# Performance work log

Measured on AMD Instinct MI355X. Metric: run time of the kernel, lower is better.

The kernel has to match this reference:

```python
import jax, jax.numpy as jnp
import numpy as np
from jax import lax

B, IN_C, DIM, HEADS, K = 8, 64, 128, 4, 3
H, W = 96, 96
HEAD_DIM = DIM // HEADS
SCALE = HEAD_DIM ** -0.5
EPS = 1e-5  # BatchNorm eps (eval mode, running_mean=0, running_var=1)


def _conv3x3(x, w):
    return lax.conv_general_dilated(x, w, (1, 1), ((1, 1), (1, 1)),
                                    dimension_numbers=('NCHW', 'OIHW', 'NCHW'))


def _cbr(x, w, g, b):
    y = _conv3x3(x, w)
    y = y * (g / jnp.sqrt(1.0 + EPS))[None, :, None, None] + b[None, :, None, None]
    return jax.nn.relu(y)


def setup_inputs() -> dict:
    key = jax.random.key(0)
    ks = jax.random.split(key, 24)
    n = lambda i, s, sc=0.05: jax.random.normal(ks[i], s, jnp.float32) * sc
    u = lambda i, s: jax.random.uniform(ks[i], s, jnp.float32, 0.5, 1.5)
    return dict(
        x=jax.random.normal(ks[0], (B, IN_C, H, W), jnp.float32),
        fg=jax.random.normal(ks[1], (B, DIM, H, W), jnp.float32),
        conv1_w=n(2, (DIM, IN_C, 3, 3)), bn1_g=u(3, (DIM,)), bn1_b=n(4, (DIM,)),
        conv2_w=n(5, (DIM, DIM, 3, 3)), bn2_g=u(6, (DIM,)), bn2_b=n(7, (DIM,)),
        v_w=n(8, (DIM, DIM)), v_b=n(9, (DIM,)),
        attn_w=n(10, (K ** 4 * HEADS, DIM)), attn_b=n(11, (K ** 4 * HEADS,)),
        proj_w=n(12, (DIM, DIM)), proj_b=n(13, (DIM,)),
        conv3_w=n(14, (DIM, DIM, 3, 3)), bn3_g=u(15, (DIM,)), bn3_b=n(16, (DIM,)),
        conv4_w=n(17, (DIM, DIM, 3, 3)), bn4_g=u(18, (DIM,)), bn4_b=n(19, (DIM,)),
    )


def reference(x, fg, conv1_w, bn1_g, bn1_b, conv2_w, bn2_g, bn2_b,
              v_w, v_b, attn_w, attn_b, proj_w, proj_b,
              conv3_w, bn3_g, bn3_b, conv4_w, bn4_g, bn4_b):
    L = H * W
    # input_cbr: two conv3x3 + BN(eval) + ReLU
    xf = _cbr(_cbr(x, conv1_w, bn1_g, bn1_b), conv2_w, bn2_g, bn2_b)  # (B,DIM,H,W)
    xh = xf.transpose(0, 2, 3, 1)                 # (B,H,W,DIM)
    fgh = fg.transpose(0, 2, 3, 1)                # (B,H,W,DIM)
    # value projection then unfold (im2col, channel-major patch ordering like torch)
    v = (xh @ v_w.T + v_b).transpose(0, 3, 1, 2)  # (B,DIM,H,W)
    patches = lax.conv_general_dilated_patches(v, (K, K), (1, 1), ((1, 1), (1, 1)))  # (B,DIM*9,H,W)
    vp = patches.reshape(B, HEADS, HEAD_DIM, K * K, L).transpose(0, 1, 4, 3, 2)  # (B,h,L,9,hd)
    # attention logits directly from fg (stride=1 -> AvgPool identity)
    attn = (fgh @ attn_w.T + attn_b).reshape(B, L, HEADS, K * K, K * K)
    attn = attn.transpose(0, 2, 1, 3, 4) * SCALE  # (B,h,L,9,9)
    attn = jax.nn.softmax(attn, axis=-1)
    # batched small matmuls: (9,9) @ (9,hd) per window
    xw = jnp.einsum('bhlpq,bhlqd->bhlpd', attn, vp)  # (B,h,L,9,hd)
    xw = xw.transpose(0, 1, 4, 3, 2).reshape(B, DIM, K, K, H, W)  # channel-major, then (kh,kw)
    # fold: overlapping scatter-add back to (H,W)
    canvas = jnp.zeros((B, DIM, H + 2, W + 2), xw.dtype)
    for ki in range(K):
        for kj in range(K):
            canvas = canvas.at[:, :, ki:ki + H, kj:kj + W].add(xw[:, :, ki, kj])
    folded = canvas[:, :, 1:H + 1, 1:W + 1]        # crop padding
    p = (folded.transpose(0, 2, 3, 1) @ proj_w.T + proj_b).transpose(0, 3, 1, 2)
    # output_cbr
    out = _cbr(_cbr(p, conv3_w, bn3_g, bn3_b), conv4_w, bn4_g, bn4_b)
    return out
```

## Files before the change

### kernel.cpp

```cpp
#include <hip/hip_runtime.h>
#include <math.h>

typedef __attribute__((ext_vector_type(8))) short short8;
typedef __attribute__((ext_vector_type(4))) float f32x4;
typedef unsigned short u16;
typedef unsigned int u32;

#define HW   96
#define LPIX 9216
static constexpr float kScale = 0.17677669529663687f;

__device__ inline u16 f2bf(float f) {
    u32 x = __float_as_uint(f);
    return (u16)((x + 0x7fffu + ((x >> 16) & 1u)) >> 16);
}
__device__ inline float bf2f(u16 v) { return __uint_as_float((u32)v << 16); }

typedef __attribute__((address_space(1))) const void gas_t;
typedef __attribute__((address_space(3))) void las_t;
__device__ __forceinline__ void g2lds16(const void* g, void* l) {
    __builtin_amdgcn_global_load_lds((gas_t*)g, (las_t*)l, 16, 0, 0);
}

template <int C>
__global__ __launch_bounds__(256) void cast_nchw_nhwc(
    const float* __restrict__ in, u16* __restrict__ out)
{
    const int y = blockIdx.x, b = blockIdx.y, tid = threadIdx.x;
    __shared__ float sT[HW * C];
    for (int i = tid; i < HW * C; i += 256) {
        int c = i / HW, xx = i - c * HW;
        sT[xx * C + c] = in[(((size_t)b * C + c) * HW + y) * HW + xx];
    }
    __syncthreads();
    for (int i = tid; i < HW * (C / 8); i += 256) {
        int c8 = i % (C / 8), xx = i / (C / 8);
        union { short8 v8; u16 u[8]; } pk;
#pragma unroll
        for (int j = 0; j < 8; ++j) pk.u[j] = f2bf(sT[xx * C + c8 * 8 + j]);
        *(short8*)&out[(((size_t)b * HW + y) * HW + xx) * C + c8 * 8] = pk.v8;
    }
}

__global__ void cast_conv_w(const float* __restrict__ w, u16* __restrict__ wp, int CIN)
{
    int n = 9 * CIN * 128;
    int i = blockIdx.x * 256 + threadIdx.x;
    if (i >= n) return;
    int NC = CIN >> 5;
    int e  = i & 7;
    int gr = i >> 3;
    int cc = gr / 2304;
    int gi = gr - cc * 2304;
    int coh = cc / NC, c = cc - coh * NC;
    int f = gi >> 8;
    int m = (gi >> 2) & 63;
    int s = gi & 3;
    int qq = (s - (m >> 1)) & 3;
    int co = coh * 64 + m;
    int ci = c * 32 + qq * 8 + e;
    wp[i] = f2bf(w[(size_t)(co * CIN + ci) * 9 + f]);
}

__global__ void cast_mat(const float* __restrict__ in, u16* __restrict__ out, int n)
{
    int i = blockIdx.x * 256 + threadIdx.x;
    if (i < n) out[i] = f2bf(in[i]);
}

template <int CIN, bool OUT_F32>
__global__ __launch_bounds__(192, 2) void conv_gemm(
    const u16* __restrict__ in, const u16* __restrict__ wp,
    const float* __restrict__ g, const float* __restrict__ be, void* outv)
{
    constexpr int NC    = CIN / 32;
    constexpr int WBYT  = 36864;
    constexpr int NHG   = 1928;

    const int bx  = blockIdx.x;
    const int b   = blockIdx.y;
    const int coh = bx >> 5;
    const int gg  = bx & 31;
    const int gsw = (gg & 7) * 4 + (gg >> 3);
    const int y0  = gsw * 3;
    const int l0h = y0 * 96 - 97;

    const int tid = threadIdx.x, lane = tid & 63, wv = tid >> 6;
    const int lx = lane & 15, q = lane >> 4;

    __shared__ __align__(16) char smem[WBYT + NHG * 16];
    float* sT = (float*)smem;

    const int aoff = lx * 64 + (((q + (lx >> 1)) & 3) << 4);
    const int pb   = wv * 96 + lx;

    f32x4 acc[4][6];
#pragma unroll
    for (int mt = 0; mt < 4; ++mt)
#pragma unroll
        for (int nt = 0; nt < 6; ++nt) acc[mt][nt] = (f32x4){0.f, 0.f, 0.f, 0.f};

    const u16* inb = in + (size_t)b * LPIX * CIN;

#pragma unroll
    for (int c = 0; c < NC; ++c) {
        if (c) __syncthreads();

        {
            const u16* wqb = wp + ((size_t)(coh * NC + c)) * 2304 * 8;
#pragma unroll
            for (int j = 0; j < 12; ++j) {
                int gj = j * 192 + tid;
                g2lds16(&wqb[(size_t)gj * 8],
                        (char*)smem + (j * 192 + wv * 64) * 16);
            }
        }
#pragma unroll
        for (int i = 0; i < 11; ++i) {
            int gi = i * 192 + tid;
            if (gi < NHG) {
                int p = gi >> 2, s = gi & 3;
                int qq = (s - (p >> 1)) & 3;
                int lh = l0h + p;
                lh = lh < 0 ? 0 : (lh >= LPIX ? LPIX - 1 : lh);
                g2lds16(&inb[(size_t)lh * CIN + c * 32 + qq * 8],
                        (char*)smem + WBYT + (i * 192 + wv * 64) * 16);
            }
        }
        asm volatile("s_waitcnt vmcnt(0)" ::: "memory");
        __builtin_amdgcn_s_barrier();
        asm volatile("" ::: "memory");

#pragma unroll
        for (int f = 0; f < 9; ++f) {
            const int dy = f / 3 - 1, dx = f % 3 - 1;
            const int off = dy * 96 + dx + 97;
            const bool vy = (unsigned)(y0 + wv + dy) < 96u;
            short8 af[4], bfr[6];
#pragma unroll
            for (int mt = 0; mt < 4; ++mt)
                af[mt] = *(const short8*)((const char*)smem + f * 4096 + mt * 1024 + aoff);
#pragma unroll
            for (int nt = 0; nt < 6; ++nt) {
                int p = pb + nt * 16 + off;
                int slot = (q + (p >> 1)) & 3;
                short8 t8 = *(const short8*)((const char*)smem + WBYT + p * 64 + slot * 16);
                bool ok = vy & ((unsigned)(nt * 16 + lx + dx) < 96u);
                bfr[nt] = ok ? t8 : (short8){0, 0, 0, 0, 0, 0, 0, 0};
            }
#pragma unroll
            for (int mt = 0; mt < 4; ++mt)
#pragma unroll
                for (int nt = 0; nt < 6; ++nt)
                    acc[mt][nt] = __builtin_amdgcn_mfma_f32_16x16x32_bf16(
                        af[mt], bfr[nt], acc[mt][nt], 0, 0, 0);
        }
    }

    const float rs = rsqrtf(1.f + 1e-5f);
    if (OUT_F32) {
        float* out = (float*)outv;
#pragma unroll
        for (int mt = 0; mt < 4; ++mt) {
#pragma unroll
            for (int reg = 0; reg < 4; ++reg) {
                int co = coh * 64 + mt * 16 + q * 4 + reg;
                float sc = g[co] * rs, bb = be[co];
#pragma unroll
                for (int nt = 0; nt < 6; ++nt) {
                    int l = (y0 + wv) * 96 + nt * 16 + lx;
                    out[((size_t)b * 128 + co) * LPIX + l] =
                        fmaxf(fmaf(acc[mt][nt][reg], sc, bb), 0.f);
                }
            }
        }
    } else {
        u16* out = (u16*)outv;
#pragma unroll
        for (int hh = 0; hh < 2; ++hh) {
            __syncthreads();
#pragma unroll
            for (int mt = 0; mt < 4; ++mt)
#pragma unroll
                for (int nn = 0; nn < 3; ++nn) {
                    int nt = hh * 3 + nn;
#pragma unroll
                    for (int reg = 0; reg < 4; ++reg)
                        sT[(wv * 48 + nn * 16 + lx) * 65 + mt * 16 + q * 4 + reg] =
                            acc[mt][nt][reg];
                }
            __syncthreads();
            for (int i = tid; i < 1152; i += 192) {
                int cog = i & 7, pxl = i >> 3;
                int wrr = pxl / 48, ofs = pxl - wrr * 48;
                int l = (y0 + wrr) * 96 + hh * 48 + ofs;
                union { short8 v8; u16 u[8]; } pk;
#pragma unroll
                for (int j = 0; j < 8; ++j) {
                    int co = coh * 64 + cog * 8 + j;
                    pk.u[j] = f2bf(fmaxf(fmaf(sT[pxl * 65 + cog * 8 + j], g[co] * rs, be[co]), 0.f));
                }
                *(short8*)&out[((size_t)b * LPIX + l) * 128 + coh * 64 + cog * 8] = pk.v8;
            }
        }
    }
}

__global__ __launch_bounds__(256) void linear_mfma(
    const u16* __restrict__ in, const u16* __restrict__ wp,
    const float* __restrict__ bias, u16* __restrict__ out)
{
    const int l0 = blockIdx.x * 64;
    const int tid = threadIdx.x, lane = tid & 63, wv = tid >> 6;
    const int wm = wv >> 1, wn = wv & 1;
    const int lx = lane & 15, q = lane >> 4;

    __shared__ char smem[4 * 64 * 40 * 2 + 4 * 128 * 40 * 2];
    u16* sX = (u16*)smem;
    u16* sW = (u16*)(smem + 4 * 64 * 40 * 2);
    float* sT = (float*)smem;

    for (int i = tid; i < 1024; i += 256) {
        int k8 = i & 15, px = i >> 4;
        short8 v = *(const short8*)&in[((size_t)(l0 + px)) * 128 + k8 * 8];
        *(short8*)&sX[((k8 >> 2) * 64 + px) * 40 + (k8 & 3) * 8] = v;
    }
    for (int i = tid; i < 2048; i += 256) {
        int k8 = i & 15, co = i >> 4;
        short8 v = *(const short8*)&wp[(size_t)co * 128 + k8 * 8];
        *(short8*)&sW[((k8 >> 2) * 128 + co) * 40 + (k8 & 3) * 8] = v;
    }
    __syncthreads();

    f32x4 acc[4][2];
#pragma unroll
    for (int mt = 0; mt < 4; ++mt)
#pragma unroll
        for (int nt = 0; nt < 2; ++nt) acc[mt][nt] = (f32x4){0.f, 0.f, 0.f, 0.f};

#pragma unroll
    for (int c4 = 0; c4 < 4; ++c4) {
        short8 af[4], bfr[2];
#pragma unroll
        for (int mt = 0; mt < 4; ++mt)
            af[mt] = *(const short8*)&sW[(c4 * 128 + wm * 64 + mt * 16 + lx) * 40 + q * 8];
#pragma unroll
        for (int nt = 0; nt < 2; ++nt)
            bfr[nt] = *(const short8*)&sX[(c4 * 64 + wn * 32 + nt * 16 + lx) * 40 + q * 8];
#pragma unroll
        for (int mt = 0; mt < 4; ++mt)
#pragma unroll
            for (int nt = 0; nt < 2; ++nt)
                acc[mt][nt] = __builtin_amdgcn_mfma_f32_16x16x32_bf16(
                    af[mt], bfr[nt], acc[mt][nt], 0, 0, 0);
    }

    for (int mh = 0; mh < 2; ++mh) {
        __syncthreads();
        if (wm == mh) {
#pragma unroll
            for (int mt = 0; mt < 4; ++mt)
#pragma unroll
                for (int nt = 0; nt < 2; ++nt)
#pragma unroll
                    for (int reg = 0; reg < 4; ++reg)
                        sT[(wn * 32 + nt * 16 + lx) * 65 + mt * 16 + q * 4 + reg] =
                            acc[mt][nt][reg];
        }
        __syncthreads();
        for (int i = tid; i < 512; i += 256) {
            int cog = i & 7, px = i >> 3;
            union { short8 v8; u16 u[8]; } pk;
#pragma unroll
            for (int j = 0; j < 8; ++j) {
                int co = mh * 64 + cog * 8 + j;
                pk.u[j] = f2bf(sT[px * 65 + cog * 8 + j] + bias[co]);
            }
            *(short8*)&out[((size_t)(l0 + px)) * 128 + mh * 64 + cog * 8] = pk.v8;
        }
    }
}

__global__ __launch_bounds__(256) void attn_mfma(
    const u16* __restrict__ fgb, const u16* __restrict__ awb,
    const float* __restrict__ ab, u16* __restrict__ A)
{
    const int lt = blockIdx.x, h = blockIdx.y, b = blockIdx.z;
    const int l0 = lt * 64;
    const int tid = threadIdx.x, lane = tid & 63, wv = tid >> 6;
    const int lx = lane & 15, q = lane >> 4;

    __shared__ char smem[4 * 64 * 40 * 2 + 4 * 96 * 40 * 2];
    u16* sX = (u16*)smem;
    u16* sW = (u16*)(smem + 4 * 64 * 40 * 2);
    float* sL = (float*)smem;

    for (int i = tid; i < 1024; i += 256) {
        int k8 = i & 15, px = i >> 4;
        short8 v = *(const short8*)&fgb[((size_t)b * LPIX + l0 + px) * 128 + k8 * 8];
        *(short8*)&sX[((k8 >> 2) * 64 + px) * 40 + (k8 & 3) * 8] = v;
    }
    for (int i = tid; i < 1536; i += 256) {
        int k8 = i & 15, rr = i >> 4;
        short8 v = {0, 0, 0, 0, 0, 0, 0, 0};
        if (rr < 81)
            v = *(const short8*)&awb[(size_t)(h * 81 + rr) * 128 + k8 * 8];
        *(short8*)&sW[((k8 >> 2) * 96 + rr) * 40 + (k8 & 3) * 8] = v;
    }
    __syncthreads();

    f32x4 acc[6];
#pragma unroll
    for (int j = 0; j < 6; ++j) acc[j] = (f32x4){0.f, 0.f, 0.f, 0.f};

#pragma unroll
    for (int c4 = 0; c4 < 4; ++c4) {
        short8 af = *(const short8*)&sX[(c4 * 64 + wv * 16 + lx) * 40 + q * 8];
#pragma unroll
        for (int j = 0; j < 6; ++j) {
            short8 bfr = *(const short8*)&sW[(c4 * 96 + j * 16 + lx) * 40 + q * 8];
            acc[j] = __builtin_amdgcn_mfma_f32_16x16x32_bf16(af, bfr, acc[j], 0, 0, 0);
        }
    }

    __syncthreads();
#pragma unroll
    for (int j = 0; j < 6; ++j)
#pragma unroll
        for (int reg = 0; reg < 4; ++reg)
            sL[(wv * 16 + q * 4 + reg) * 97 + j * 16 + lx] = acc[j][reg];
    __syncthreads();

    for (int t = tid; t < 576; t += 256) {
        int px = t & 63, p = t >> 6;
        const int rbase = h * 81 + p * 9;
        float lg[9], m = -1e30f;
#pragma unroll
        for (int qq = 0; qq < 9; ++qq) {
            lg[qq] = (sL[px * 97 + p * 9 + qq] + ab[rbase + qq]) * kScale;
            m = fmaxf(m, lg[qq]);
        }
        float s = 0.f;
#pragma unroll
        for (int qq = 0; qq < 9; ++qq) { lg[qq] = __expf(lg[qq] - m); s += lg[qq]; }
        float inv = 1.f / s;
        u16* Ab = &A[(((size_t)(b * 4 + h) * 9 + p) * 9) * LPIX + l0 + px];
#pragma unroll
        for (int qq = 0; qq < 9; ++qq) Ab[(size_t)qq * LPIX] = f2bf(lg[qq] * inv);
    }
}

__global__ __launch_bounds__(384, 4) void attn_fold(
    const u16* __restrict__ A, const u16* __restrict__ v,
    u16* __restrict__ out)
{
    const int yt = blockIdx.x, h = blockIdx.y, b = blockIdx.z;
    const int y0 = yt * 4;
    const int tid = threadIdx.x;
    const int yl  = tid / 96;
    const int x   = tid - yl * 96;
    const int y   = y0 + yl;
    const int l   = y * 96 + x;

    __shared__ u16 sV[8 * 96 * 32];

    const u16* vb = v + (size_t)b * LPIX * 128 + h * 32;
    for (int t = tid; t < 3072; t += 384) {
        int k = t & 3, s = t >> 2;
        int r = s / 96, xx = s - r * 96;
        int gy = y0 - 2 + r;
        uint4 uu = make_uint4(0u, 0u, 0u, 0u);
        if ((unsigned)gy < 96u)
            uu = *(const uint4*)&vb[(size_t)(gy * 96 + xx) * 128 + k * 8];
        *(uint4*)&sV[(size_t)s * 32 + k * 8] = uu;
    }

    float S[25];
#pragma unroll
    for (int i = 0; i < 25; ++i) S[i] = 0.f;

    const u16* Ab = A + ((size_t)(b * 4 + h) * 81) * (size_t)LPIX;
#pragma unroll
    for (int ki = 0; ki < 3; ++ki) {
        const int ly = y + 1 - ki;
        const bool vy = ((unsigned)ly < 96u);
#pragma unroll
        for (int kj = 0; kj < 3; ++kj) {
            const int lx2 = x + 1 - kj;
            if (vy && (unsigned)lx2 < 96u) {
                const u16* Ap = Ab + (size_t)(ki * 3 + kj) * 9 * (size_t)LPIX
                              + (ly * 96 + lx2);
#pragma unroll
                for (int qq = 0; qq < 9; ++qq) {
                    const int qi = qq / 3, qj = qq - qi * 3;
                    S[(qi - ki + 2) * 5 + (qj - kj + 2)] += bf2f(Ap[(size_t)qq * LPIX]);
                }
            }
        }
    }

    __syncthreads();

    float acc[32];
#pragma unroll
    for (int c = 0; c < 32; ++c) acc[c] = 0.f;

#pragma unroll
    for (int oy = 0; oy < 5; ++oy) {
        const int r = yl + oy;
#pragma unroll
        for (int ox = 0; ox < 5; ++ox) {
            const int xx = x + ox - 2;
            if ((unsigned)xx >= 96u) continue;
            const float sc = S[oy * 5 + ox];
            const u16* vp = &sV[(size_t)(r * 96 + xx) * 32];
#pragma unroll
            for (int c8 = 0; c8 < 4; ++c8) {
                const uint4 uu = *(const uint4*)&vp[c8 * 8];
                acc[c8 * 8 + 0] = fmaf(sc, __uint_as_float(uu.x << 16),          acc[c8 * 8 + 0]);
                acc[c8 * 8 + 1] = fmaf(sc, __uint_as_float(uu.x & 0xffff0000u), acc[c8 * 8 + 1]);
                acc[c8 * 8 + 2] = fmaf(sc, __uint_as_float(uu.y << 16),          acc[c8 * 8 + 2]);
                acc[c8 * 8 + 3] = fmaf(sc, __uint_as_float(uu.y & 0xffff0000u), acc[c8 * 8 + 3]);
                acc[c8 * 8 + 4] = fmaf(sc, __uint_as_float(uu.z << 16),          acc[c8 * 8 + 4]);
                acc[c8 * 8 + 5] = fmaf(sc, __uint_as_float(uu.z & 0xffff0000u), acc[c8 * 8 + 5]);
                acc[c8 * 8 + 6] = fmaf(sc, __uint_as_float(uu.w << 16),          acc[c8 * 8 + 6]);
                acc[c8 * 8 + 7] = fmaf(sc, __uint_as_float(uu.w & 0xffff0000u), acc[c8 * 8 + 7]);
            }
        }
    }

    u16* ob = &out[((size_t)b * LPIX + l) * 128 + h * 32];
#pragma unroll
    for (int gidx = 0; gidx < 4; ++gidx) {
        union { short8 v8; u16 u[8]; } pk;
#pragma unroll
        for (int j = 0; j < 8; ++j) pk.u[j] = f2bf(acc[gidx * 8 + j]);
        *(short8*)&ob[gidx * 8] = pk.v8;
    }
}

extern "C" void kernel_launch(void* const* d_in, const int* in_sizes, int n_in,
                              void* d_out, int out_size, void* d_ws, size_t ws_size,
                              hipStream_t stream)
{
    const float* x    = (const float*)d_in[0];
    const float* fg   = (const float*)d_in[1];
    const float* c1w  = (const float*)d_in[2];
    const float* bn1g = (const float*)d_in[3];
    const float* bn1b = (const float*)d_in[4];
    const float* c2w  = (const float*)d_in[5];
    const float* bn2g = (const float*)d_in[6];
    const float* bn2b = (const float*)d_in[7];
    const float* vw   = (const float*)d_in[8];
    const float* vb   = (const float*)d_in[9];
    const float* aw   = (const float*)d_in[10];
    const float* abv  = (const float*)d_in[11];
    const float* pw   = (const float*)d_in[12];
    const float* pb   = (const float*)d_in[13];
    const float* c3w  = (const float*)d_in[14];
    const float* bn3g = (const float*)d_in[15];
    const float* bn3b = (const float*)d_in[16];
    const float* c4w  = (const float*)d_in[17];
    const float* bn4g = (const float*)d_in[18];
    const float* bn4b = (const float*)d_in[19];

    char* wsp = (char*)d_ws;
    size_t off = 0;
    auto carve = [&](size_t bytes) {
        void* pp = wsp + off;
        off += (bytes + 255) & ~(size_t)255;
        return pp;
    };
    u16*   xb   = (u16*)carve((size_t)8 * LPIX * 64 * 2);
    u16*   fgb  = (u16*)carve((size_t)8 * LPIX * 128 * 2);
    u16*   actA = (u16*)carve((size_t)8 * LPIX * 128 * 2);
    u16*   actB = (u16*)carve((size_t)8 * LPIX * 128 * 2);
    u16*   Abuf = (u16*)carve((size_t)8 * 324 * LPIX * 2);
    u16*   w1p  = (u16*)carve((size_t)9 * 2 * 128 * 32 * 2);
    u16*   w2p  = (u16*)carve((size_t)9 * 4 * 128 * 32 * 2);
    u16*   w3p  = (u16*)carve((size_t)9 * 4 * 128 * 32 * 2);
    u16*   w4p  = (u16*)carve((size_t)9 * 4 * 128 * 32 * 2);
    u16*   vwp  = (u16*)carve((size_t)128 * 128 * 2);
    u16*   pwp  = (u16*)carve((size_t)128 * 128 * 2);
    u16*   awb  = (u16*)carve((size_t)324 * 128 * 2);

    cast_nchw_nhwc<64><<<dim3(HW, 8), 256, 0, stream>>>(x, xb);
    cast_nchw_nhwc<128><<<dim3(HW, 8), 256, 0, stream>>>(fg, fgb);
    cast_conv_w<<<(9 * 64 * 128 + 255) / 256, 256, 0, stream>>>(c1w, w1p, 64);
    cast_conv_w<<<(9 * 128 * 128 + 255) / 256, 256, 0, stream>>>(c2w, w2p, 128);
    cast_conv_w<<<(9 * 128 * 128 + 255) / 256, 256, 0, stream>>>(c3w, w3p, 128);
    cast_conv_w<<<(9 * 128 * 128 + 255) / 256, 256, 0, stream>>>(c4w, w4p, 128);
    cast_mat<<<(16384 + 255) / 256, 256, 0, stream>>>(vw, vwp, 16384);
    cast_mat<<<(16384 + 255) / 256, 256, 0, stream>>>(pw, pwp, 16384);
    cast_mat<<<(324 * 128 + 255) / 256, 256, 0, stream>>>(aw, awb, 324 * 128);

    conv_gemm<64, false><<<dim3(64, 8), 192, 0, stream>>>(xb, w1p, bn1g, bn1b, actA);
    conv_gemm<128, false><<<dim3(64, 8), 192, 0, stream>>>(actA, w2p, bn2g, bn2b, actB);
    linear_mfma<<<1152, 256, 0, stream>>>(actB, vwp, vb, actA);
    attn_mfma<<<dim3(144, 4, 8), 256, 0, stream>>>(fgb, awb, abv, Abuf);
    attn_fold<<<dim3(24, 4, 8), 384, 0, stream>>>(Abuf, actA, actB);
    linear_mfma<<<1152, 256, 0, stream>>>(actB, pwp, pb, actA);
    conv_gemm<128, false><<<dim3(64, 8), 192, 0, stream>>>(actA, w3p, bn3g, bn3b, actB);
    conv_gemm<128, true><<<dim3(64, 8), 192, 0, stream>>>(actB, w4p, bn4g, bn4b, d_out);
}
```

Baseline: 368.2 us.

## Enlarge attn_mfma pixel tile to 128 with async LDS loads and swizzled weights

The attention-logit kernel now processes 128 pixels per block instead of 64, so each block reuses its loaded weights across twice as many pixels and the grid is halved. Global-to-LDS copies now use direct global_load_lds with an XOR-style swizzled layout instead of register-staged padded copies. A new kernel pre-packs the attention weights into that swizzled, zero-padded layout. LDS use rises to 56KB per block and the accumulators double, which may reduce occupancy.

```diff
diff --git a/kernel.cpp b/kernel.cpp
--- a/kernel.cpp
+++ b/kernel.cpp
@@ -62,6 +62,21 @@
     wp[i] = f2bf(w[(size_t)(co * CIN + ci) * 9 + f]);
 }
 
+__global__ void cast_attn_w(const float* __restrict__ aw, u16* __restrict__ wp)
+{
+    int i = blockIdx.x * 256 + threadIdx.x;
+    if (i >= 4 * 1536 * 8) return;
+    int e = i & 7;
+    int g = i >> 3;
+    int h = g / 1536, r = g - h * 1536;
+    int c4 = r / 384, r2 = r - c4 * 384;
+    int rr = r2 >> 2, s = r2 & 3;
+    int qq = (s - (rr >> 1)) & 3;
+    int ci = c4 * 32 + qq * 8 + e;
+    float v = (rr < 81) ? aw[(size_t)(h * 81 + rr) * 128 + ci] : 0.f;
+    wp[i] = f2bf(v);
+}
+
 __global__ void cast_mat(const float* __restrict__ in, u16* __restrict__ out, int n)
 {
     int i = blockIdx.x * 256 + threadIdx.x;
@@ -281,58 +296,79 @@
     }
 }
 
-__global__ __launch_bounds__(256) void attn_mfma(
-    const u16* __restrict__ fgb, const u16* __restrict__ awb,
+__global__ __launch_bounds__(256, 2) void attn_mfma(
+    const u16* __restrict__ fgb, const u16* __restrict__ awp,
     const float* __restrict__ ab, u16* __restrict__ A)
 {
     const int lt = blockIdx.x, h = blockIdx.y, b = blockIdx.z;
-    const int l0 = lt * 64;
+    const int l0 = lt * 128;
     const int tid = threadIdx.x, lane = tid & 63, wv = tid >> 6;
     const int lx = lane & 15, q = lane >> 4;
 
-    __shared__ char smem[4 * 64 * 40 * 2 + 4 * 96 * 40 * 2];
-    u16* sX = (u16*)smem;
-    u16* sW = (u16*)(smem + 4 * 64 * 40 * 2);
+    __shared__ __align__(16) char smem[57344];
     float* sL = (float*)smem;
 
-    for (int i = tid; i < 1024; i += 256) {
-        int k8 = i & 15, px = i >> 4;
-        short8 v = *(const short8*)&fgb[((size_t)b * LPIX + l0 + px) * 128 + k8 * 8];
-        *(short8*)&sX[((k8 >> 2) * 64 + px) * 40 + (k8 & 3) * 8] = v;
-    }
-    for (int i = tid; i < 1536; i += 256) {
-        int k8 = i & 15, rr = i >> 4;
-        short8 v = {0, 0, 0, 0, 0, 0, 0, 0};
-        if (rr < 81)
-            v = *(const short8*)&awb[(size_t)(h * 81 + rr) * 128 + k8 * 8];
-        *(short8*)&sW[((k8 >> 2) * 96 + rr) * 40 + (k8 & 3) * 8] = v;
-    }
+    const u16* fb = fgb + ((size_t)b * LPIX + l0) * 128;
+#pragma unroll
+    for (int i = 0; i < 8; ++i) {
+        int gg = i * 256 + tid;
+        int c4 = gg >> 9, r = gg & 511, px = r >> 2, s = r & 3;
+        int qq = (s - (px >> 1)) & 3;
+        g2lds16(&fb[(size_t)px * 128 + c4 * 32 + qq * 8],
+                (char*)smem + (i * 256 + wv * 64) * 16);
+    }
+    const u16* wb = awp + (size_t)h * 1536 * 8;
+#pragma unroll
+    for (int i = 0; i < 6; ++i) {
+        g2lds16(&wb[(size_t)(i * 256 + tid) * 8],
+                (char*)smem + 32768 + (i * 256 + wv * 64) * 16);
+    }
+    asm volatile("s_waitcnt vmcnt(0)" ::: "memory");
+    __builtin_amdgcn_s_barrier();
+    asm volatile("" ::: "memory");
+
+    f32x4 acc[2][6];
+#pragma unroll
+    for (int nt = 0; nt < 2; ++nt)
+#pragma unroll
+        for (int j = 0; j < 6; ++j) acc[nt][j] = (f32x4){0.f, 0.f, 0.f, 0.f};
+
+#pragma unroll
+    for (int c4 = 0; c4 < 4; ++c4) {
+        short8 af[2], bfr[6];
+#pragma unroll
+        for (int nt = 0; nt < 2; ++nt) {
+            int px = wv * 32 + nt * 16 + lx;
+            af[nt] = *(const short8*)((const char*)smem + c4 * 8192 + px * 64
+                                      + (((q + (px >> 1)) & 3) << 4));
+        }
+#pragma unroll
+        for (int j = 0; j < 6; ++j) {
+            int rr = j * 16 + lx;
+            bfr[j] = *(const short8*)((const char*)smem + 32768 + c4 * 6144 + rr * 64
+                                      + (((q + (rr >> 1)) & 3) << 4));
+        }
+#pragma unroll
+        for (int nt = 0; nt < 2; ++nt)
+#pragma unroll
+            for (int j = 0; j < 6; ++j)
+                acc[nt][j] = __builtin_amdgcn_mfma_f32_16x16x32_bf16(
+                    af[nt], bfr[j], acc[nt][j], 0, 0, 0);
+    }
+
     __syncthreads();
-
-    f32x4 acc[6];
-#pragma unroll
-    for (int j = 0; j < 6; ++j) acc[j] = (f32x4){0.f, 0.f, 0.f, 0.f};
-
-#pragma unroll
-    for (int c4 = 0; c4 < 4; ++c4) {
-        short8 af = *(const short8*)&sX[(c4 * 64 + wv * 16 + lx) * 40 + q * 8];
-#pragma unroll
-        for (int j = 0; j < 6; ++j) {
-            short8 bfr = *(const short8*)&sW[(c4 * 96 + j * 16 + lx) * 40 + q * 8];
-            acc[j] = __builtin_amdgcn_mfma_f32_16x16x32_bf16(af, bfr, acc[j], 0, 0, 0);
-        }
-    }
-
+#pragma unroll
+    for (int nt = 0; nt < 2; ++nt)
+#pragma unroll
+        for (int j = 0; j < 6; ++j)
+#pragma unroll
+            for (int reg = 0; reg < 4; ++reg)
+                sL[(wv * 32 + nt * 16 + q * 4 + reg) * 97 + j * 16 + lx] =
+                    acc[nt][j][reg];
     __syncthreads();
-#pragma unroll
-    for (int j = 0; j < 6; ++j)
-#pragma unroll
-        for (int reg = 0; reg < 4; ++reg)
-            sL[(wv * 16 + q * 4 + reg) * 97 + j * 16 + lx] = acc[j][reg];
-    __syncthreads();
-
-    for (int t = tid; t < 576; t += 256) {
-        int px = t & 63, p = t >> 6;
+
+    for (int t = tid; t < 1152; t += 256) {
+        int px = t & 127, p = t >> 7;
         const int rbase = h * 81 + p * 9;
         float lg[9], m = -1e30f;
 #pragma unroll
@@ -482,7 +518,7 @@
     u16*   w4p  = (u16*)carve((size_t)9 * 4 * 128 * 32 * 2);
     u16*   vwp  = (u16*)carve((size_t)128 * 128 * 2);
     u16*   pwp  = (u16*)carve((size_t)128 * 128 * 2);
-    u16*   awb  = (u16*)carve((size_t)324 * 128 * 2);
+    u16*   awp  = (u16*)carve((size_t)4 * 1536 * 8 * 2);
 
     cast_nchw_nhwc<64><<<dim3(HW, 8), 256, 0, stream>>>(x, xb);
     cast_nchw_nhwc<128><<<dim3(HW, 8), 256, 0, stream>>>(fg, fgb);
@@ -492,12 +528,12 @@
     cast_conv_w<<<(9 * 128 * 128 + 255) / 256, 256, 0, stream>>>(c4w, w4p, 128);
     cast_mat<<<(16384 + 255) / 256, 256, 0, stream>>>(vw, vwp, 16384);
     cast_mat<<<(16384 + 255) / 256, 256, 0, stream>>>(pw, pwp, 16384);
-    cast_mat<<<(324 * 128 + 255) / 256, 256, 0, stream>>>(aw, awb, 324 * 128);
+    cast_attn_w<<<192, 256, 0, stream>>>(aw, awp);
 
     conv_gemm<64, false><<<dim3(64, 8), 192, 0, stream>>>(xb, w1p, bn1g, bn1b, actA);
     conv_gemm<128, false><<<dim3(64, 8), 192, 0, stream>>>(actA, w2p, bn2g, bn2b, actB);
     linear_mfma<<<1152, 256, 0, stream>>>(actB, vwp, vb, actA);
-    attn_mfma<<<dim3(144, 4, 8), 256, 0, stream>>>(fgb, awb, abv, Abuf);
+    attn_mfma<<<dim3(72, 4, 8), 256, 0, stream>>>(fgb, awp, abv, Abuf);
     attn_fold<<<dim3(24, 4, 8), 384, 0, stream>>>(Abuf, actA, actB);
     linear_mfma<<<1152, 256, 0, stream>>>(actB, pwp, pb, actA);
     conv_gemm<128, false><<<dim3(64, 8), 192, 0, stream>>>(actA, w3p, bn3g, bn3b, actB);
```

Result: slower. 476.4 us (+29.4%).
